# Optimization experiments

Hardware: AMD Instinct MI355X
Metric: run time of the kernel (lower is better)

## Reference

```python
import jax, jax.numpy as jnp
import numpy as np

STAGE = 100
EPS = 1e-5


def bin_affine(w, shift_aff, sign_aff):
    """Vectorized equivalent of the 100-iteration range-mask loop.
    Original: for i in range(stage): mask = (w >= lo_i) & (w < hi_i);
              shift += w.detach()*shift_aff[i]*mask; sign += w.detach()*sign_aff[i]*mask.
    Equivalent to bucketize + gather + scale. Element equal to w.max() falls
    outside every half-open bin (strict <), so it gets zero, matching torch.
    w is detached in the original, so gradients flow only to the affines.
    """
    wf = w.reshape(-1)
    wmin, wmax = wf.min(), wf.max()
    t = (wf - wmin) / (wmax - wmin) * STAGE
    idx = jnp.floor(t).astype(jnp.int32)
    valid = (idx >= 0) & (idx < STAGE)
    idxc = jnp.clip(idx, 0, STAGE - 1)
    wd = jax.lax.stop_gradient(wf)
    shift = jnp.where(valid, wd * shift_aff[idxc], 0.0)
    sign = jnp.where(valid, wd * sign_aff[idxc], 0.0)
    return shift.reshape(w.shape), sign.reshape(w.shape)


def eff_weight(w, shift_aff, sign_aff):
    # Conv2dShift forward with externally-assigned continuous shift/sign:
    # effective weight = sign * 2**shift (deepshift-style, unrounded).
    shift, sign = bin_affine(w, shift_aff, sign_aff)
    return sign * jnp.exp2(shift)


def conv2d(x, w, stride=1, pad=0, groups=1):
    return jax.lax.conv_general_dilated(
        x, w, (stride, stride), [(pad, pad), (pad, pad)],
        dimension_numbers=("NCHW", "OIHW", "NCHW"), feature_group_count=groups)


def batchnorm(x, g, b):
    m = x.mean((0, 2, 3), keepdims=True)
    v = x.var((0, 2, 3), keepdims=True)
    return (x - m) * jax.lax.rsqrt(v + EPS) * g[None, :, None, None] + b[None, :, None, None]


def setup_inputs() -> dict:
    key = jax.random.key(0)
    ks = jax.random.split(key, 16)
    d = {
        "x": jax.random.normal(ks[0], (32, 256, 56, 56), jnp.float32),
        "w_ds": 0.05 * jax.random.normal(ks[1], (512, 256, 1, 1), jnp.float32),
        "w_c1": 0.05 * jax.random.normal(ks[2], (128, 256, 1, 1), jnp.float32),
        "w_peg": 0.05 * jax.random.normal(ks[3], (128, 1, 3, 3), jnp.float32),
        "w_c2": 0.05 * jax.random.normal(ks[4], (128, 128, 3, 3), jnp.float32),
        "w_c3": 0.05 * jax.random.normal(ks[5], (512, 128, 1, 1), jnp.float32),
        "aff_ds_shift": jax.random.normal(ks[6], (STAGE,), jnp.float32),
        "aff_ds_sign": jax.random.normal(ks[7], (STAGE,), jnp.float32),
        "aff_c1_shift": jax.random.normal(ks[8], (STAGE,), jnp.float32),
        "aff_c1_sign": jax.random.normal(ks[9], (STAGE,), jnp.float32),
        "aff_c2_shift": jax.random.normal(ks[10], (STAGE,), jnp.float32),
        "aff_c2_sign": jax.random.normal(ks[11], (STAGE,), jnp.float32),
        "aff_c3_shift": jax.random.normal(ks[12], (STAGE,), jnp.float32),
        "aff_c3_sign": jax.random.normal(ks[13], (STAGE,), jnp.float32),
        "g_bn_ds": jnp.ones((512,), jnp.float32),
        "b_bn_ds": jnp.zeros((512,), jnp.float32),
        "g_bn1": jnp.ones((128,), jnp.float32),
        "b_bn1": jnp.zeros((128,), jnp.float32),
        "g_bn2": jnp.ones((128,), jnp.float32),
        "b_bn2": jnp.zeros((128,), jnp.float32),
        "g_bn3": jnp.ones((512,), jnp.float32),
        "b_bn3": jnp.zeros((512,), jnp.float32),
    }
    return d


def reference(x, w_ds, w_c1, w_peg, w_c2, w_c3,
              aff_ds_shift, aff_ds_sign, aff_c1_shift, aff_c1_sign,
              aff_c2_shift, aff_c2_sign, aff_c3_shift, aff_c3_sign,
              g_bn_ds, b_bn_ds, g_bn1, b_bn1, g_bn2, b_bn2, g_bn3, b_bn3):
    # main branch (fmap_size == self.fmap_size): bin downsample + conv1/2/3 weights
    wds_e = eff_weight(w_ds, aff_ds_shift, aff_ds_sign)
    wc1_e = eff_weight(w_c1, aff_c1_shift, aff_c1_sign)
    wc2_e = eff_weight(w_c2, aff_c2_shift, aff_c2_sign)
    wc3_e = eff_weight(w_c3, aff_c3_shift, aff_c3_sign)

    # downsample = Conv1x1 -> BN -> ReLU
    residual = jax.nn.relu(batchnorm(conv2d(x, wds_e), g_bn_ds, b_bn_ds))

    h = conv2d(x, wc1_e)                                   # 1x1, 256->128
    h = conv2d(h, w_peg, stride=1, pad=1, groups=128)      # PEG depthwise 3x3
    h = jax.nn.relu(batchnorm(h, g_bn1, b_bn1))            # bn1 + act1
    h = conv2d(h, wc2_e, stride=1, pad=1)                  # 3x3, 128->128
    h = jax.nn.relu(batchnorm(h, g_bn2, b_bn2))            # bn2 + act2
    h = conv2d(h, wc3_e)                                   # 1x1, 128->512
    h = batchnorm(h, g_bn3, b_bn3)                         # bn3
    return jax.nn.relu(h + residual)                       # act3
```

## Files before the change

### kernel.cpp

```cpp
#include <hip/hip_runtime.h>
#include <stdint.h>


#define HW    3136
#define WID   56
#define NB    32
#define FLIP_TENSOR 1

#define OFF_MM    0
#define OFF_SC1   8
#define OFF_BI1   136
#define OFF_SC2   264
#define OFF_BI2   392
#define OFF_SC3   520
#define OFF_BI3   1032
#define OFF_SCDS  1544
#define OFF_BIDS  2056
#define WB_BASE_BYTES 16384ULL
#define WB_M  0ULL
#define WB_C2 163840ULL
#define WB_C3 311296ULL
#define PS1S_B  786432ULL
#define PS1Q_B  802816ULL
#define PS2S_B  819200ULL
#define PS2Q_B  1622016ULL
#define PS3S_B  2424832ULL
#define PS3Q_B  5636096ULL
#define PSDS_B  8847360ULL
#define PSDQ_B  12058624ULL
#define AC_BASE_BYTES 16777216ULL
#define AC_A 0ULL
#define AC_B 12845056ULL
#define AC_C 25690112ULL
#define AC_R 77070336ULL
#define AC_XT AC_C
#define NSLOT 1568

typedef __attribute__((ext_vector_type(8))) short bfrag8;
typedef __attribute__((ext_vector_type(4))) float facc4;

__device__ __forceinline__ unsigned short f2bf(float f) {
  unsigned u = __float_as_uint(f);
  u = u + 0x7FFFu + ((u >> 16) & 1u);
  return (unsigned short)(u >> 16);
}
__device__ __forceinline__ float bf2f(unsigned short h) {
  return __uint_as_float(((unsigned)h) << 16);
}
__device__ __forceinline__ unsigned fmap(float f) {
  unsigned u = __float_as_uint(f);
  return (u & 0x80000000u) ? ~u : (u | 0x80000000u);
}
__device__ __forceinline__ float funmap(unsigned m) {
  unsigned u = (m & 0x80000000u) ? (m & 0x7FFFFFFFu) : ~m;
  return __uint_as_float(u);
}

__device__ __forceinline__ void gload_lds16(const void* g, void* l) {
  __builtin_amdgcn_global_load_lds(
      (const __attribute__((address_space(1))) unsigned int*)g,
      (__attribute__((address_space(3))) unsigned int*)l,
      16, 0, 0);
}

__global__ void k_mm_init(unsigned* mm) {
  int t = threadIdx.x;
  if (t < 4) { mm[2 * t] = 0xFFFFFFFFu; mm[2 * t + 1] = 0u; }
}

__device__ __forceinline__ void tensor_of(int g0, int& tensor, int& local0) {
  if (g0 < 131072)      { tensor = 0; local0 = g0; }
  else if (g0 < 163840) { tensor = 1; local0 = g0 - 131072; }
  else if (g0 < 311296) { tensor = 2; local0 = g0 - 163840; }
  else                  { tensor = 3; local0 = g0 - 311296; }
}

__global__ __launch_bounds__(256) void k_minmax(
    const float* __restrict__ w_ds, const float* __restrict__ w_c1,
    const float* __restrict__ w_c2, const float* __restrict__ w_c3,
    unsigned* __restrict__ mm) {
  __shared__ unsigned smin[256], smax[256];
  int t = threadIdx.x;
  int tensor, local0;
  tensor_of(blockIdx.x * 1024, tensor, local0);
  const float* src = (tensor == 0) ? w_ds : (tensor == 1) ? w_c1 : (tensor == 2) ? w_c2 : w_c3;
  float4 v = *(const float4*)(src + local0 + t * 4);
  unsigned mn, mx;
  {
    unsigned m0 = fmap(v.x), m1 = fmap(v.y), m2 = fmap(v.z), m3 = fmap(v.w);
    mn = min(min(m0, m1), min(m2, m3));
    mx = max(max(m0, m1), max(m2, m3));
  }
  smin[t] = mn; smax[t] = mx;
  __syncthreads();
  for (int s = 128; s > 0; s >>= 1) {
    if (t < s) { smin[t] = min(smin[t], smin[t + s]); smax[t] = max(smax[t], smax[t + s]); }
    __syncthreads();
  }
  if (t == 0) {
    atomicMin(&mm[2 * tensor], smin[0]);
    atomicMax(&mm[2 * tensor + 1], smax[0]);
  }
}

__global__ __launch_bounds__(256) void k_effw(
    const float* __restrict__ w_ds, const float* __restrict__ w_c1,
    const float* __restrict__ w_c2, const float* __restrict__ w_c3,
    const float* __restrict__ sh_ds, const float* __restrict__ sg_ds,
    const float* __restrict__ sh_c1, const float* __restrict__ sg_c1,
    const float* __restrict__ sh_c2, const float* __restrict__ sg_c2,
    const float* __restrict__ sh_c3, const float* __restrict__ sg_c3,
    const unsigned* __restrict__ mm, unsigned short* __restrict__ wb) {
  int t = threadIdx.x;
  int tensor, local0;
  tensor_of(blockIdx.x * 1024, tensor, local0);
  const float* src = (tensor == 0) ? w_ds : (tensor == 1) ? w_c1 : (tensor == 2) ? w_c2 : w_c3;
  const float* sha = (tensor == 0) ? sh_ds : (tensor == 1) ? sh_c1 : (tensor == 2) ? sh_c2 : sh_c3;
  const float* sga = (tensor == 0) ? sg_ds : (tensor == 1) ? sg_c1 : (tensor == 2) ? sg_c2 : sg_c3;
  float wmin = funmap(mm[2 * tensor]);
  float wmax = funmap(mm[2 * tensor + 1]);
  float rng = __fsub_rn(wmax, wmin);
  float I32 = __fdiv_rn(rng, 100.0f);
  float edge100 = __fadd_rn(wmin, __fmul_rn(100.0f, I32));
  bool s32 = (wmax < edge100);
  bool binmax = (tensor == FLIP_TENSOR) ? !s32 : s32;
  float4 v4 = *(const float4*)(src + local0 + t * 4);
  float vs[4] = {v4.x, v4.y, v4.z, v4.w};
#pragma unroll
  for (int e = 0; e < 4; ++e) {
    int l = local0 + t * 4 + e;
    float v = vs[e];
    float ew;
    if (v == wmax) {
      ew = binmax ? (v * sga[99]) * exp2f(v * sha[99]) : 0.0f;
    } else {
      float tt = __fmul_rn(__fdiv_rn(__fsub_rn(v, wmin), rng), 100.0f);
      int idx = (int)floorf(tt);
      bool valid = (idx >= 0) && (idx < 100);
      int ic = valid ? idx : 0;
      float shift = valid ? v * sha[ic] : 0.0f;
      float sign  = valid ? v * sga[ic] : 0.0f;
      ew = sign * exp2f(shift);
    }
    unsigned short h = f2bf(ew);
    if (tensor == 0) {
      int co = l >> 8, ci = l & 255;
      wb[WB_M + (size_t)(128 + co) * 256 + ci] = h;
    } else if (tensor == 1) {
      int co = l >> 8, ci = l & 255;
      wb[WB_M + (size_t)co * 256 + ci] = h;
    } else if (tensor == 2) {
      int co = l / 1152; int r2 = l - co * 1152;
      int ci = r2 / 9; int tap = r2 - ci * 9;
      wb[WB_C2 + (size_t)co * 1152 + tap * 128 + ci] = h;
    } else {
      int co = l >> 7, ci = l & 127;
      wb[WB_C3 + (size_t)co * 128 + ci] = h;
    }
  }
}

__global__ __launch_bounds__(256) void k_tr(
    const float* __restrict__ x, unsigned short* __restrict__ XT) {
  __shared__ short lt[64 * 258];
  int bid = blockIdx.x;
  int sp_blk = bid % 49, n = bid / 49;
  int s0 = sp_blk * 64;
  int t = threadIdx.x;
  {
    const float* row = x + ((size_t)n * 256 + t) * HW + s0;
#pragma unroll
    for (int i = 0; i < 16; ++i) {
      float4 v = *(const float4*)(row + i * 4);
      lt[(i * 4 + 0) * 258 + t] = (short)f2bf(v.x);
      lt[(i * 4 + 1) * 258 + t] = (short)f2bf(v.y);
      lt[(i * 4 + 2) * 258 + t] = (short)f2bf(v.z);
      lt[(i * 4 + 3) * 258 + t] = (short)f2bf(v.w);
    }
  }
  __syncthreads();
  {
    int spi = t >> 2, cb = (t & 3) * 64;
    unsigned short* dst = XT + ((size_t)n * HW + s0 + spi) * 256 + cb;
    const short* srcl = &lt[spi * 258 + cb];
#pragma unroll
    for (int q = 0; q < 8; ++q)
      *(float4*)((short*)dst + q * 8) = *(const float4*)(srcl + q * 8);
  }
}

__global__ __launch_bounds__(256) void k_mconvG(
    const unsigned short* __restrict__ XT, const unsigned short* __restrict__ Wt,
    unsigned short* __restrict__ Y1, unsigned short* __restrict__ Y2,
    float* __restrict__ PS, float* __restrict__ PQ) {
  __shared__ short lx[64 * 128];
  __shared__ float redS[128][2], redQ[128][2];
  const int tid  = threadIdx.x;
  const int lane = tid & 63;
  const int wv   = tid >> 6;
  int lid = blockIdx.x;
  int xcd = lid & 7;
  int j   = lid >> 3;
  int co_blk = j % 5;
  int t_  = xcd * 196 + j / 5;
  int sp_blk = t_ % 49;
  int n      = t_ / 49;
  const int s0  = sp_blk * 64;
  const int co0 = co_blk * 128;
  const size_t nsp0 = (size_t)n * HW + s0;

  const int wco  = (wv >> 1) * 64;
  const int wsp  = (wv & 1) * 32;
  const int lrow = lane & 15;
  const int lkg  = lane >> 4;
  const int kb8  = lkg * 8;

  int spl[2];
#pragma unroll
  for (int nn = 0; nn < 2; ++nn) spl[nn] = wsp + nn * 16 + lrow;

  facc4 acc[4][2];
#pragma unroll
  for (int m = 0; m < 4; ++m)
#pragma unroll
    for (int nn = 0; nn < 2; ++nn) acc[m][nn] = (facc4)(0.0f);

#pragma unroll
  for (int ph = 0; ph < 2; ++ph) {
    const int k0 = ph * 128;
    __syncthreads();
#pragma unroll
    for (int i = 0; i < 4; ++i) {
      int B  = tid * 16 + i * 4096;
      int sp = B >> 8;
      int p  = (B >> 4) & 15;
      int c  = p ^ (sp & 7);
      const unsigned short* g = XT + (nsp0 + sp) * 256 + k0 + c * 8;
      gload_lds16(g, (char*)lx + B);
    }
    __syncthreads();
    bfrag8 af[4][4];
#pragma unroll
    for (int kk = 0; kk < 4; ++kk)
#pragma unroll
      for (int m = 0; m < 4; ++m)
        af[kk][m] = *(const bfrag8*)(Wt +
            (size_t)(co0 + wco + m * 16 + lrow) * 256 + k0 + kk * 32 + kb8);
#pragma unroll
    for (int kk = 0; kk < 4; ++kk) {
#pragma unroll
      for (int nn = 0; nn < 2; ++nn) {
        int row = spl[nn];
        int chunk = (kk * 4 + lkg) ^ (row & 7);
        bfrag8 b = *(const bfrag8*)((const char*)lx + row * 256 + (chunk << 4));
#pragma unroll
        for (int m = 0; m < 4; ++m)
          acc[m][nn] = __builtin_amdgcn_mfma_f32_16x16x32_bf16(
              af[kk][m], b, acc[m][nn], 0, 0, 0);
      }
    }
  }
  {
    unsigned short* Yb;
    int coL, COst;
    if (co0 < 128) { Yb = Y1; coL = co0; COst = 128; }
    else           { Yb = Y2; coL = co0 - 128; COst = 512; }
#pragma unroll
    for (int m = 0; m < 4; ++m)
#pragma unroll
      for (int nn = 0; nn < 2; ++nn)
#pragma unroll
        for (int r = 0; r < 4; ++r) {
          int co_g = coL + wco + m * 16 + lkg * 4 + r;
          int sp_g = s0 + wsp + nn * 16 + lrow;
          Yb[((size_t)n * COst + co_g) * HW + sp_g] = f2bf(acc[m][nn][r]);
        }
  }
  if (co0 >= 128) {
#pragma unroll
    for (int m = 0; m < 4; ++m)
#pragma unroll
      for (int r = 0; r < 4; ++r) {
        float sv = acc[m][0][r] + acc[m][1][r];
        float qv = acc[m][0][r] * acc[m][0][r] + acc[m][1][r] * acc[m][1][r];
#pragma unroll
        for (int d = 1; d < 16; d <<= 1) {
          sv += __shfl_xor(sv, d);
          qv += __shfl_xor(qv, d);
        }
        if (lrow == 0) {
          int col = wco + m * 16 + lkg * 4 + r;
          redS[col][wv & 1] = sv;
          redQ[col][wv & 1] = qv;
        }
      }
    __syncthreads();
    if (tid < 128) {
      int cstat = co0 - 128 + tid;
      int slot = n * 49 + sp_blk;
      PS[(size_t)cstat * NSLOT + slot] = redS[tid][0] + redS[tid][1];
      PQ[(size_t)cstat * NSLOT + slot] = redQ[tid][0] + redQ[tid][1];
    }
  }
}

template <int CI, int TAPS, int KBLK, int COOUT, bool XBF,
          bool FUSEIN, bool STATS, int NCOB>
__global__ __launch_bounds__(256) void k_mconv6(
    const void* __restrict__ Xv, const unsigned short* __restrict__ Wt,
    unsigned short* __restrict__ Y1,
    const float* __restrict__ fsc, const float* __restrict__ fbi,
    float* __restrict__ PS, float* __restrict__ PQ) {
  constexpr int NSP = (TAPS == 9) ? 192 : 64;
  constexpr int ST  = KBLK + 2;
  __shared__ short lx[NSP][ST];
  __shared__ float redS[128][2], redQ[128][2];
  const int tid  = threadIdx.x;
  const int lane = tid & 63;
  const int wv   = tid >> 6;
  int lid = blockIdx.x;
  int xcd = lid & 7;
  int j   = lid >> 3;
  int co_blk = j % NCOB;
  int t_  = xcd * 196 + j / NCOB;
  int sp_blk = t_ % 49;
  int n      = t_ / 49;
  const int s0  = sp_blk * 64;
  const int co0 = co_blk * 128;
  const int NK  = CI * TAPS;
  const unsigned short* Xh = (const unsigned short*)Xv + (size_t)n * CI * HW;
  const float*          Xf = (const float*)Xv + (size_t)n * CI * HW;

  const int wco  = (wv >> 1) * 64;
  const int wsp  = (wv & 1) * 32;
  const int lrow = lane & 15;
  const int lkg  = lane >> 4;
  const int kb8  = lkg * 8;

  int spl[2], yc[2], xc[2];
#pragma unroll
  for (int nn = 0; nn < 2; ++nn) {
    spl[nn] = wsp + nn * 16 + lrow;
    int s = s0 + spl[nn];
    yc[nn] = s / WID;
    xc[nn] = s - yc[nn] * WID;
  }

  facc4 acc[4][2];
#pragma unroll
  for (int m = 0; m < 4; ++m)
#pragma unroll
    for (int nn = 0; nn < 2; ++nn) acc[m][nn] = (facc4)(0.0f);

  for (int k0 = 0; k0 < CI; k0 += KBLK) {
    __syncthreads();
    if (TAPS == 9) {
#pragma unroll
      for (int i = 0; i < 3; ++i) {
        int task = tid + i * 256;
        int spi = task % 192;
        int kc  = task / 192;
        int p = s0 - 64 + spi;
        short v[8];
        if ((unsigned)p < (unsigned)HW) {
          const unsigned short* pp = Xh + (size_t)(k0 + kc * 8) * HW + p;
#pragma unroll
          for (int jj = 0; jj < 8; ++jj) {
            if (FUSEIN) {
              float f = bf2f(pp[(size_t)jj * HW]);
              f = fmaxf(fmaf(f, fsc[k0 + kc * 8 + jj], fbi[k0 + kc * 8 + jj]), 0.0f);
              v[jj] = (short)f2bf(f);
            } else {
              v[jj] = (short)pp[(size_t)jj * HW];
            }
          }
        } else {
#pragma unroll
          for (int jj = 0; jj < 8; ++jj) v[jj] = 0;
        }
        *(short4*)(&lx[spi][kc * 8])     = (short4){v[0], v[1], v[2], v[3]};
        *(short4*)(&lx[spi][kc * 8 + 4]) = (short4){v[4], v[5], v[6], v[7]};
      }
    } else {
#pragma unroll
      for (int i = 0; i < KBLK / 32; ++i) {
        int task = tid + i * 256;
        int spi = task & 63;
        int kc  = task >> 6;
        int p = s0 + spi;
        short v[8];
        if (XBF) {
          const unsigned short* pp = Xh + (size_t)(k0 + kc * 8) * HW + p;
#pragma unroll
          for (int jj = 0; jj < 8; ++jj) {
            if (FUSEIN) {
              float f = bf2f(pp[(size_t)jj * HW]);
              f = fmaxf(fmaf(f, fsc[k0 + kc * 8 + jj], fbi[k0 + kc * 8 + jj]), 0.0f);
              v[jj] = (short)f2bf(f);
            } else {
              v[jj] = (short)pp[(size_t)jj * HW];
            }
          }
        } else {
          const float* pf = Xf + (size_t)(k0 + kc * 8) * HW + p;
#pragma unroll
          for (int jj = 0; jj < 8; ++jj) v[jj] = (short)f2bf(pf[(size_t)jj * HW]);
        }
        *(short4*)(&lx[spi][kc * 8])     = (short4){v[0], v[1], v[2], v[3]};
        *(short4*)(&lx[spi][kc * 8 + 4]) = (short4){v[4], v[5], v[6], v[7]};
      }
    }
    __syncthreads();
    if (TAPS == 1) {
      bfrag8 af[KBLK / 32][4];
#pragma unroll
      for (int kk = 0; kk < KBLK / 32; ++kk)
#pragma unroll
        for (int m = 0; m < 4; ++m)
          af[kk][m] = *(const bfrag8*)(Wt +
              (size_t)(co0 + wco + m * 16 + lrow) * NK + k0 + kk * 32 + kb8);
#pragma unroll
      for (int kk = 0; kk < KBLK / 32; ++kk) {
#pragma unroll
        for (int nn = 0; nn < 2; ++nn) {
          bfrag8 b = *(const bfrag8*)(&lx[spl[nn]][kk * 32 + kb8]);
#pragma unroll
          for (int m = 0; m < 4; ++m)
            acc[m][nn] = __builtin_amdgcn_mfma_f32_16x16x32_bf16(
                af[kk][m], b, acc[m][nn], 0, 0, 0);
        }
      }
    } else {
      bfrag8 afc[4], afn[4];
#pragma unroll
      for (int m = 0; m < 4; ++m)
        afc[m] = *(const bfrag8*)(Wt +
            (size_t)(co0 + wco + m * 16 + lrow) * NK + k0 + kb8);
      for (int tap = 0; tap < 9; ++tap) {
        if (tap < 8) {
#pragma unroll
          for (int m = 0; m < 4; ++m)
            afn[m] = *(const bfrag8*)(Wt +
                (size_t)(co0 + wco + m * 16 + lrow) * NK + (tap + 1) * CI + k0 + kb8);
        }
        const int dy = tap / 3 - 1;
        const int dx = tap % 3 - 1;
        const int off = dy * WID + dx;
#pragma unroll
        for (int nn = 0; nn < 2; ++nn) {
          bfrag8 b = *(const bfrag8*)(&lx[64 + spl[nn] + off][kb8]);
          bool valid = ((unsigned)(xc[nn] + dx) < (unsigned)WID) &&
                       ((unsigned)(yc[nn] + dy) < (unsigned)WID);
          if (!valid) b = (bfrag8)(short)0;
#pragma unroll
          for (int m = 0; m < 4; ++m)
            acc[m][nn] = __builtin_amdgcn_mfma_f32_16x16x32_bf16(
                afc[m], b, acc[m][nn], 0, 0, 0);
        }
#pragma unroll
        for (int m = 0; m < 4; ++m) afc[m] = afn[m];
      }
    }
  }
#pragma unroll
  for (int m = 0; m < 4; ++m)
#pragma unroll
    for (int nn = 0; nn < 2; ++nn)
#pragma unroll
      for (int r = 0; r < 4; ++r) {
        int co_g = co0 + wco + m * 16 + lkg * 4 + r;
        int sp_g = s0 + wsp + nn * 16 + lrow;
        Y1[((size_t)n * COOUT + co_g) * HW + sp_g] = f2bf(acc[m][nn][r]);
      }
  if (STATS) {
#pragma unroll
    for (int m = 0; m < 4; ++m)
#pragma unroll
      for (int r = 0; r < 4; ++r) {
        float sv = acc[m][0][r] + acc[m][1][r];
        float qv = acc[m][0][r] * acc[m][0][r] + acc[m][1][r] * acc[m][1][r];
#pragma unroll
        for (int d = 1; d < 16; d <<= 1) {
          sv += __shfl_xor(sv, d);
          qv += __shfl_xor(qv, d);
        }
        if (lrow == 0) {
          int col = wco + m * 16 + lkg * 4 + r;
          redS[col][wv & 1] = sv;
          redQ[col][wv & 1] = qv;
        }
      }
    __syncthreads();
    if (tid < 128) {
      int cstat = co0 + tid;
      int slot = n * 49 + sp_blk;
      PS[(size_t)cstat * NSLOT + slot] = redS[tid][0] + redS[tid][1];
      PQ[(size_t)cstat * NSLOT + slot] = redQ[tid][0] + redQ[tid][1];
    }
  }
}

__global__ __launch_bounds__(256) void k_dw(
    const unsigned short* __restrict__ Xin, const float* __restrict__ wp,
    unsigned short* __restrict__ Yout,
    float* __restrict__ PS, float* __restrict__ PQ) {
  __shared__ float pl[HW];
  __shared__ float rs[256], rq[256];
  int bid = blockIdx.x;
  int c = bid & 127;
  int n = bid >> 7;
  const unsigned short* src = Xin + (size_t)bid * HW;
  int t = threadIdx.x;
  for (int q = t; q < HW / 4; q += 256) {
    ushort4 h4 = *(const ushort4*)(src + q * 4);
    pl[q * 4 + 0] = bf2f(h4.x); pl[q * 4 + 1] = bf2f(h4.y);
    pl[q * 4 + 2] = bf2f(h4.z); pl[q * 4 + 3] = bf2f(h4.w);
  }
  float w[9];
#pragma unroll
  for (int k = 0; k < 9; ++k) w[k] = wp[c * 9 + k];
  __syncthreads();
  unsigned short* dst = Yout + (size_t)bid * HW;
  float accS = 0.0f, accQ = 0.0f;
  for (int q = t; q < HW / 4; q += 256) {
    float o[4];
#pragma unroll
    for (int e = 0; e < 4; ++e) {
      int s = q * 4 + e;
      int y = s / WID, xcc = s - y * WID;
      float accv = 0.0f;
#pragma unroll
      for (int ky = 0; ky < 3; ++ky) {
        int yy = y + ky - 1;
        if (yy < 0 || yy >= WID) continue;
#pragma unroll
        for (int kx = 0; kx < 3; ++kx) {
          int xx = xcc + kx - 1;
          if (xx < 0 || xx >= WID) continue;
          accv = fmaf(w[ky * 3 + kx], pl[yy * WID + xx], accv);
        }
      }
      o[e] = accv;
      accS += accv;
      accQ = fmaf(accv, accv, accQ);
    }
    ushort4 ov;
    ov.x = f2bf(o[0]); ov.y = f2bf(o[1]); ov.z = f2bf(o[2]); ov.w = f2bf(o[3]);
    *(ushort4*)(dst + q * 4) = ov;
  }
  rs[t] = accS; rq[t] = accQ;
  __syncthreads();
  for (int st = 128; st > 0; st >>= 1) {
    if (t < st) { rs[t] += rs[t + st]; rq[t] += rq[t + st]; }
    __syncthreads();
  }
  if (t == 0) {
    PS[(size_t)c * NB + n] = rs[0];
    PQ[(size_t)c * NB + n] = rq[0];
  }
}

__global__ __launch_bounds__(256) void k_red(
    const float* __restrict__ S, const float* __restrict__ Q,
    const float* __restrict__ g, const float* __restrict__ b,
    float* __restrict__ sc_o, float* __restrict__ bi_o, int npart) {
  int c = blockIdx.x, t = threadIdx.x;
  double s = 0.0, q = 0.0;
  for (int i = t; i < npart; i += 256) {
    s += S[(size_t)c * npart + i];
    q += Q[(size_t)c * npart + i];
  }
  __shared__ double ss[256], qq[256];
  ss[t] = s; qq[t] = q;
  __syncthreads();
  for (int st = 128; st > 0; st >>= 1) {
    if (t < st) { ss[t] += ss[t + st]; qq[t] += qq[t + st]; }
    __syncthreads();
  }
  if (t == 0) {
    double nn = (double)HW * NB;
    double mean = ss[0] / nn;
    double var = qq[0] / nn - mean * mean;
    float rstd = (float)(1.0 / sqrt(var + 1e-5));
    float sc = g[c] * rstd;
    sc_o[c] = sc;
    bi_o[c] = b[c] - (float)mean * sc;
  }
}

__global__ __launch_bounds__(256) void k_final(
    float* __restrict__ out, const unsigned short* __restrict__ hC,
    const unsigned short* __restrict__ r,
    const float* __restrict__ sc3, const float* __restrict__ bi3,
    const float* __restrict__ scds, const float* __restrict__ bids) {
  const int QPN = 512 * 784;
  const int total = NB * QPN;
  for (int q = blockIdx.x * 256 + threadIdx.x; q < total; q += gridDim.x * 256) {
    int qn = q % QPN;
    int c = qn / 784;
    ushort4 hh = *(const ushort4*)(hC + (size_t)q * 4);
    ushort4 rh = *(const ushort4*)(r + (size_t)q * 4);
    float s3 = sc3[c], b3 = bi3[c], sd = scds[c], bd = bids[c];
    float4 o;
    float rb;
    rb = fmaxf(fmaf(bf2f(rh.x), sd, bd), 0.0f); o.x = fmaxf(fmaf(bf2f(hh.x), s3, b3) + rb, 0.0f);
    rb = fmaxf(fmaf(bf2f(rh.y), sd, bd), 0.0f); o.y = fmaxf(fmaf(bf2f(hh.y), s3, b3) + rb, 0.0f);
    rb = fmaxf(fmaf(bf2f(rh.z), sd, bd), 0.0f); o.z = fmaxf(fmaf(bf2f(hh.z), s3, b3) + rb, 0.0f);
    rb = fmaxf(fmaf(bf2f(rh.w), sd, bd), 0.0f); o.w = fmaxf(fmaf(bf2f(hh.w), s3, b3) + rb, 0.0f);
    *(float4*)(out + (size_t)q * 4) = o;
  }
}

extern "C" void kernel_launch(void* const* d_in, const int* in_sizes, int n_in,
                              void* d_out, int out_size, void* d_ws, size_t ws_size,
                              hipStream_t stream) {
  const float *x = nullptr, *w_ds = nullptr, *w_c1 = nullptr, *w_peg = nullptr,
              *w_c2 = nullptr, *w_c3 = nullptr;
  const float* aff[8] = {nullptr};
  const float* v512[4] = {nullptr};
  const float* v128[4] = {nullptr};
  int naff = 0, n512 = 0, n128 = 0;
  for (int i = 0; i < n_in; ++i) {
    const float* p = (const float*)d_in[i];
    switch (in_sizes[i]) {
      case 25690112: x = p; break;
      case 131072:   w_ds = p; break;
      case 32768:    w_c1 = p; break;
      case 1152:     w_peg = p; break;
      case 147456:   w_c2 = p; break;
      case 65536:    w_c3 = p; break;
      case 100:      if (naff < 8) aff[naff++] = p; break;
      case 512:      if (n512 < 4) v512[n512++] = p; break;
      case 128:      if (n128 < 4) v128[n128++] = p; break;
      default: break;
    }
  }
  const float *a_ds_sh = aff[0], *a_ds_sg = aff[1], *a_c1_sh = aff[2], *a_c1_sg = aff[3];
  const float *a_c2_sh = aff[4], *a_c2_sg = aff[5], *a_c3_sh = aff[6], *a_c3_sg = aff[7];
  const float *g_ds = v512[0], *b_ds = v512[1], *g3 = v512[2], *b3 = v512[3];
  const float *g1 = v128[0], *b1 = v128[1], *g2 = v128[2], *b2 = v128[3];

  float* ws  = (float*)d_ws;
  float* out = (float*)d_out;
  unsigned* mm = (unsigned*)(ws + OFF_MM);
  unsigned short* wb = (unsigned short*)((char*)d_ws + WB_BASE_BYTES);
  unsigned short* ac = (unsigned short*)((char*)d_ws + AC_BASE_BYTES);
  unsigned short* bufA  = ac + AC_A;
  unsigned short* bufB  = ac + AC_B;
  unsigned short* bufC  = ac + AC_C;
  unsigned short* bufR  = ac + AC_R;
  unsigned short* bufXT = ac + AC_XT;
  float* ps1S = (float*)((char*)d_ws + PS1S_B);
  float* ps1Q = (float*)((char*)d_ws + PS1Q_B);
  float* ps2S = (float*)((char*)d_ws + PS2S_B);
  float* ps2Q = (float*)((char*)d_ws + PS2Q_B);
  float* ps3S = (float*)((char*)d_ws + PS3S_B);
  float* ps3Q = (float*)((char*)d_ws + PS3Q_B);
  float* psdS = (float*)((char*)d_ws + PSDS_B);
  float* psdQ = (float*)((char*)d_ws + PSDQ_B);

  k_mm_init<<<dim3(1), dim3(64), 0, stream>>>(mm);
  k_minmax<<<dim3(368), dim3(256), 0, stream>>>(w_ds, w_c1, w_c2, w_c3, mm);
  k_effw<<<dim3(368), dim3(256), 0, stream>>>(
      w_ds, w_c1, w_c2, w_c3,
      a_ds_sh, a_ds_sg, a_c1_sh, a_c1_sg, a_c2_sh, a_c2_sg, a_c3_sh, a_c3_sg,
      mm, wb);
  k_tr<<<dim3(1568), dim3(256), 0, stream>>>(x, bufXT);

  k_mconvG<<<dim3(7840), dim3(256), 0, stream>>>(
      bufXT, wb + WB_M, bufA, bufR, psdS, psdQ);
  k_red<<<dim3(512), dim3(256), 0, stream>>>(psdS, psdQ, g_ds, b_ds,
                                             ws + OFF_SCDS, ws + OFF_BIDS, NSLOT);
  k_dw<<<dim3(NB * 128), dim3(256), 0, stream>>>(bufA, w_peg, bufB, ps1S, ps1Q);
  k_red<<<dim3(128), dim3(256), 0, stream>>>(ps1S, ps1Q, g1, b1,
                                             ws + OFF_SC1, ws + OFF_BI1, NB);
  k_mconv6<128, 9, 32, 128, true, true, true, 1>
      <<<dim3(1568), dim3(256), 0, stream>>>(
      bufB, wb + WB_C2, bufA, ws + OFF_SC1, ws + OFF_BI1, ps2S, ps2Q);
  k_red<<<dim3(128), dim3(256), 0, stream>>>(ps2S, ps2Q, g2, b2,
                                             ws + OFF_SC2, ws + OFF_BI2, NSLOT);
  k_mconv6<128, 1, 128, 512, true, true, true, 4>
      <<<dim3(6272), dim3(256), 0, stream>>>(
      bufA, wb + WB_C3, bufC, ws + OFF_SC2, ws + OFF_BI2, ps3S, ps3Q);
  k_red<<<dim3(512), dim3(256), 0, stream>>>(ps3S, ps3Q, g3, b3,
                                             ws + OFF_SC3, ws + OFF_BI3, NSLOT);
  k_final<<<dim3(4096), dim3(256), 0, stream>>>(out, bufC, bufR,
                                                ws + OFF_SC3, ws + OFF_BI3,
                                                ws + OFF_SCDS, ws + OFF_BIDS);
}
```

Baseline: 554.3 us.

## Pre-transpose BN2-activated input to channel-last for conv3 via async LDS loads

The conv3 1x1 path previously applied BN2+ReLU on the fly while gathering channel-strided bf16 elements into LDS, once per output-channel block (four times per tile). A new kernel applies BN2+ReLU once and transposes the activation to a spatial-major, channel-contiguous layout. A new conv3 GEMM kernel then loads it with 16-byte direct global-to-LDS copies into an XOR-swizzled buffer. This adds one extra pass over the intermediate activation (write plus read) in exchange for coalesced loads and no repeated normalization work. The now-unused TAPS==1 path in the generic kernel is removed.

Result: no change. 552.9 us (-0.3%).

```diff
diff --git a/kernel.cpp b/kernel.cpp
--- a/kernel.cpp
+++ b/kernel.cpp
@@ -189,6 +189,40 @@
   }
 }
 
+__global__ __launch_bounds__(256) void k_applyT(
+    const unsigned short* __restrict__ A, const float* __restrict__ sc,
+    const float* __restrict__ bi, unsigned short* __restrict__ A2) {
+  __shared__ short lt[64 * 130];
+  int bid = blockIdx.x;
+  int sp_blk = bid % 49, n = bid / 49;
+  int s0 = sp_blk * 64;
+  int t = threadIdx.x;
+  {
+    int c = t >> 1, part = (t & 1) * 32;
+    float s = sc[c], b = bi[c];
+    const unsigned short* src = A + ((size_t)n * 128 + c) * HW + s0 + part;
+#pragma unroll
+    for (int q = 0; q < 4; ++q) {
+      float4 raw = *(const float4*)(src + q * 8);
+      const unsigned short* pv = (const unsigned short*)&raw;
+#pragma unroll
+      for (int jj = 0; jj < 8; ++jj) {
+        float f = fmaxf(fmaf(bf2f(pv[jj]), s, b), 0.0f);
+        lt[(part + q * 8 + jj) * 130 + c] = (short)f2bf(f);
+      }
+    }
+  }
+  __syncthreads();
+  {
+    int spi = t >> 2, cb = (t & 3) * 32;
+    unsigned short* dst = A2 + ((size_t)n * HW + s0 + spi) * 128 + cb;
+    const short* srcl = &lt[spi * 130 + cb];
+#pragma unroll
+    for (int q = 0; q < 4; ++q)
+      *(float4*)((short*)dst + q * 8) = *(const float4*)(srcl + q * 8);
+  }
+}
+
 __global__ __launch_bounds__(256) void k_mconvG(
     const unsigned short* __restrict__ XT, const unsigned short* __restrict__ Wt,
     unsigned short* __restrict__ Y1, unsigned short* __restrict__ Y2,
@@ -297,6 +331,110 @@
     __syncthreads();
     if (tid < 128) {
       int cstat = co0 - 128 + tid;
+      int slot = n * 49 + sp_blk;
+      PS[(size_t)cstat * NSLOT + slot] = redS[tid][0] + redS[tid][1];
+      PQ[(size_t)cstat * NSLOT + slot] = redQ[tid][0] + redQ[tid][1];
+    }
+  }
+}
+
+__global__ __launch_bounds__(256) void k_mconvG3(
+    const unsigned short* __restrict__ A2, const unsigned short* __restrict__ Wt,
+    unsigned short* __restrict__ Y,
+    float* __restrict__ PS, float* __restrict__ PQ) {
+  __shared__ short lx[64 * 128];
+  __shared__ float redS[128][2], redQ[128][2];
+  const int tid  = threadIdx.x;
+  const int lane = tid & 63;
+  const int wv   = tid >> 6;
+  int lid = blockIdx.x;
+  int xcd = lid & 7;
+  int j   = lid >> 3;
+  int co_blk = j % 4;
+  int t_  = xcd * 196 + j / 4;
+  int sp_blk = t_ % 49;
+  int n      = t_ / 49;
+  const int s0  = sp_blk * 64;
+  const int co0 = co_blk * 128;
+  const size_t nsp0 = (size_t)n * HW + s0;
+
+  const int wco  = (wv >> 1) * 64;
+  const int wsp  = (wv & 1) * 32;
+  const int lrow = lane & 15;
+  const int lkg  = lane >> 4;
+  const int kb8  = lkg * 8;
+
+  int spl[2];
+#pragma unroll
+  for (int nn = 0; nn < 2; ++nn) spl[nn] = wsp + nn * 16 + lrow;
+
+  facc4 acc[4][2];
+#pragma unroll
+  for (int m = 0; m < 4; ++m)
+#pragma unroll
+    for (int nn = 0; nn < 2; ++nn) acc[m][nn] = (facc4)(0.0f);
+
+#pragma unroll
+  for (int i = 0; i < 4; ++i) {
+    int B  = tid * 16 + i * 4096;
+    int sp = B >> 8;
+    int p  = (B >> 4) & 15;
+    int c  = p ^ (sp & 7);
+    const unsigned short* g = A2 + (nsp0 + sp) * 128 + c * 8;
+    gload_lds16(g, (char*)lx + B);
+  }
+  __syncthreads();
+  bfrag8 af[4][4];
+#pragma unroll
+  for (int kk = 0; kk < 4; ++kk)
+#pragma unroll
+    for (int m = 0; m < 4; ++m)
+      af[kk][m] = *(const bfrag8*)(Wt +
+          (size_t)(co0 + wco + m * 16 + lrow) * 128 + kk * 32 + kb8);
+#pragma unroll
+  for (int kk = 0; kk < 4; ++kk) {
+#pragma unroll
+    for (int nn = 0; nn < 2; ++nn) {
+      int row = spl[nn];
+      int chunk = (kk * 4 + lkg) ^ (row & 7);
+      bfrag8 b = *(const bfrag8*)((const char*)lx + row * 256 + (chunk << 4));
+#pragma unroll
+      for (int m = 0; m < 4; ++m)
+        acc[m][nn] = __builtin_amdgcn_mfma_f32_16x16x32_bf16(
+            af[kk][m], b, acc[m][nn], 0, 0, 0);
+    }
+  }
+#pragma unroll
+  for (int m = 0; m < 4; ++m)
+#pragma unroll
+    for (int nn = 0; nn < 2; ++nn)
+#pragma unroll
+      for (int r = 0; r < 4; ++r) {
+        int co_g = co0 + wco + m * 16 + lkg * 4 + r;
+        int sp_g = s0 + wsp + nn * 16 + lrow;
+        Y[((size_t)n * 512 + co_g) * HW + sp_g] = f2bf(acc[m][nn][r]);
+      }
+  {
+#pragma unroll
+    for (int m = 0; m < 4; ++m)
+#pragma unroll
+      for (int r = 0; r < 4; ++r) {
+        float sv = acc[m][0][r] + acc[m][1][r];
+        float qv = acc[m][0][r] * acc[m][0][r] + acc[m][1][r] * acc[m][1][r];
+#pragma unroll
+        for (int d = 1; d < 16; d <<= 1) {
+          sv += __shfl_xor(sv, d);
+          qv += __shfl_xor(qv, d);
+        }
+        if (lrow == 0) {
+          int col = wco + m * 16 + lkg * 4 + r;
+          redS[col][wv & 1] = sv;
+          redQ[col][wv & 1] = qv;
+        }
+      }
+    __syncthreads();
+    if (tid < 128) {
+      int cstat = co0 + tid;
       int slot = n * 49 + sp_blk;
       PS[(size_t)cstat * NSLOT + slot] = redS[tid][0] + redS[tid][1];
       PQ[(size_t)cstat * NSLOT + slot] = redQ[tid][0] + redQ[tid][1];
@@ -329,7 +467,6 @@
   const int co0 = co_blk * 128;
   const int NK  = CI * TAPS;
   const unsigned short* Xh = (const unsigned short*)Xv + (size_t)n * CI * HW;
-  const float*          Xf = (const float*)Xv + (size_t)n * CI * HW;
 
   const int wco  = (wv >> 1) * 64;
   const int wsp  = (wv & 1) * 32;
@@ -354,7 +491,7 @@
 
   for (int k0 = 0; k0 < CI; k0 += KBLK) {
     __syncthreads();
-    if (TAPS == 9) {
+    {
 #pragma unroll
       for (int i = 0; i < 3; ++i) {
         int task = tid + i * 256;
@@ -381,56 +518,9 @@
         *(short4*)(&lx[spi][kc * 8])     = (short4){v[0], v[1], v[2], v[3]};
         *(short4*)(&lx[spi][kc * 8 + 4]) = (short4){v[4], v[5], v[6], v[7]};
       }
-    } else {
-#pragma unroll
-      for (int i = 0; i < KBLK / 32; ++i) {
-        int task = tid + i * 256;
-        int spi = task & 63;
-        int kc  = task >> 6;
-        int p = s0 + spi;
-        short v[8];
-        if (XBF) {
-          const unsigned short* pp = Xh + (size_t)(k0 + kc * 8) * HW + p;
-#pragma unroll
-          for (int jj = 0; jj < 8; ++jj) {
-            if (FUSEIN) {
-              float f = bf2f(pp[(size_t)jj * HW]);
-              f = fmaxf(fmaf(f, fsc[k0 + kc * 8 + jj], fbi[k0 + kc * 8 + jj]), 0.0f);
-              v[jj] = (short)f2bf(f);
-            } else {
-              v[jj] = (short)pp[(size_t)jj * HW];
-            }
-          }
-        } else {
-          const float* pf = Xf + (size_t)(k0 + kc * 8) * HW + p;
-#pragma unroll
-          for (int jj = 0; jj < 8; ++jj) v[jj] = (short)f2bf(pf[(size_t)jj * HW]);
-        }
-        *(short4*)(&lx[spi][kc * 8])     = (short4){v[0], v[1], v[2], v[3]};
-        *(short4*)(&lx[spi][kc * 8 + 4]) = (short4){v[4], v[5], v[6], v[7]};
-      }
-    }
-    __syncthreads();
-    if (TAPS == 1) {
-      bfrag8 af[KBLK / 32][4];
-#pragma unroll
-      for (int kk = 0; kk < KBLK / 32; ++kk)
-#pragma unroll
-        for (int m = 0; m < 4; ++m)
-          af[kk][m] = *(const bfrag8*)(Wt +
-              (size_t)(co0 + wco + m * 16 + lrow) * NK + k0 + kk * 32 + kb8);
-#pragma unroll
-      for (int kk = 0; kk < KBLK / 32; ++kk) {
-#pragma unroll
-        for (int nn = 0; nn < 2; ++nn) {
-          bfrag8 b = *(const bfrag8*)(&lx[spl[nn]][kk * 32 + kb8]);
-#pragma unroll
-          for (int m = 0; m < 4; ++m)
-            acc[m][nn] = __builtin_amdgcn_mfma_f32_16x16x32_bf16(
-                af[kk][m], b, acc[m][nn], 0, 0, 0);
-        }
-      }
-    } else {
+    }
+    __syncthreads();
+    {
       bfrag8 afc[4], afn[4];
 #pragma unroll
       for (int m = 0; m < 4; ++m)
@@ -650,6 +740,7 @@
   unsigned short* bufC  = ac + AC_C;
   unsigned short* bufR  = ac + AC_R;
   unsigned short* bufXT = ac + AC_XT;
+  unsigned short* bufA2 = ac + AC_B;
   float* ps1S = (float*)((char*)d_ws + PS1S_B);
   float* ps1Q = (float*)((char*)d_ws + PS1Q_B);
   float* ps2S = (float*)((char*)d_ws + PS2S_B);
@@ -679,9 +770,10 @@
       bufB, wb + WB_C2, bufA, ws + OFF_SC1, ws + OFF_BI1, ps2S, ps2Q);
   k_red<<<dim3(128), dim3(256), 0, stream>>>(ps2S, ps2Q, g2, b2,
                                              ws + OFF_SC2, ws + OFF_BI2, NSLOT);
-  k_mconv6<128, 1, 128, 512, true, true, true, 4>
-      <<<dim3(6272), dim3(256), 0, stream>>>(
-      bufA, wb + WB_C3, bufC, ws + OFF_SC2, ws + OFF_BI2, ps3S, ps3Q);
+  k_applyT<<<dim3(1568), dim3(256), 0, stream>>>(bufA, ws + OFF_SC2, ws + OFF_BI2,
+                                                 bufA2);
+  k_mconvG3<<<dim3(6272), dim3(256), 0, stream>>>(
+      bufA2, wb + WB_C3, bufC, ps3S, ps3Q);
   k_red<<<dim3(512), dim3(256), 0, stream>>>(ps3S, ps3Q, g3, b3,
                                              ws + OFF_SC3, ws + OFF_BI3, NSLOT);
   k_final<<<dim3(4096), dim3(256), 0, stream>>>(out, bufC, bufR,
```
